# Optimization experiments

Hardware: AMD Instinct MI355X
Metric: run time of the kernel (lower is better)

## Reference

```python
import jax, jax.numpy as jnp
import numpy as np

N = 100000
IN_DIM = 256
HID = 64
HEADS = 2
OUT_DIM = 64
E = 1600000
NEG_SLOPE = 0.2


def gat_conv(x, edge_index, W, att_src, att_dst, bias):
    # PyG GATConv with heads=HEADS, concat=True, add_self_loops=True.
    # x: [N, IN_DIM]; edge_index: [2, E] (row0=src, row1=dst)
    loops = jnp.arange(N, dtype=edge_index.dtype)
    src = jnp.concatenate([edge_index[0], loops])  # [E+N]
    dst = jnp.concatenate([edge_index[1], loops])  # [E+N]
    h = (x @ W).reshape(N, HEADS, HID)             # [N, H, C]
    a_src = jnp.einsum('nhc,hc->nh', h, att_src)   # [N, H]
    a_dst = jnp.einsum('nhc,hc->nh', h, att_dst)   # [N, H]
    e = jax.nn.leaky_relu(a_src[src] + a_dst[dst], NEG_SLOPE)  # [E+N, H]
    # segment softmax over incoming edges of each dst node
    m = jax.ops.segment_max(e, dst, num_segments=N)            # [N, H]
    p = jnp.exp(e - m[dst])
    denom = jax.ops.segment_sum(p, dst, num_segments=N)        # [N, H]
    alpha = p / denom[dst]                                     # [E+N, H]
    msg = h[src] * alpha[:, :, None]                           # [E+N, H, C]
    out = jax.ops.segment_sum(msg, dst, num_segments=N)        # [N, H, C]
    return out.reshape(N, HEADS * HID) + bias


def setup_inputs() -> dict:
    key = jax.random.key(0)
    ks = jax.random.split(key, 12)
    s_in = 1.0 / np.sqrt(IN_DIM)
    s_h = 1.0 / np.sqrt(HID)
    s_fc = 1.0 / np.sqrt(HEADS * HID * 2)
    return {
        'x': jax.random.normal(ks[0], (N, IN_DIM), jnp.float32),
        'edge_index_connected': jax.random.randint(ks[1], (2, E), 0, N, jnp.int32),
        'edge_index_liked': jax.random.randint(ks[2], (2, E), 0, N, jnp.int32),
        'W1': jax.random.normal(ks[3], (IN_DIM, HEADS * HID), jnp.float32) * s_in,
        'att_src1': jax.random.normal(ks[4], (HEADS, HID), jnp.float32) * s_h,
        'att_dst1': jax.random.normal(ks[5], (HEADS, HID), jnp.float32) * s_h,
        'b1': jnp.zeros((HEADS * HID,), jnp.float32),
        'W2': jax.random.normal(ks[6], (IN_DIM, HEADS * HID), jnp.float32) * s_in,
        'att_src2': jax.random.normal(ks[7], (HEADS, HID), jnp.float32) * s_h,
        'att_dst2': jax.random.normal(ks[8], (HEADS, HID), jnp.float32) * s_h,
        'b2': jnp.zeros((HEADS * HID,), jnp.float32),
        'fc_W': jax.random.normal(ks[9], (HEADS * HID * 2, OUT_DIM), jnp.float32) * s_fc,
        'fc_b': jnp.zeros((OUT_DIM,), jnp.float32),
    }


def reference(x, edge_index_connected, edge_index_liked, W1, att_src1, att_dst1, b1,
              W2, att_src2, att_dst2, b2, fc_W, fc_b):
    xc = jax.nn.relu(gat_conv(x, edge_index_connected, W1, att_src1, att_dst1, b1))
    xl = jax.nn.relu(gat_conv(x, edge_index_liked, W2, att_src2, att_dst2, b2))
    x_comb = jnp.concatenate([xc, xl], axis=1)  # [N, 4*HID]
    return x_comb @ fc_W + fc_b
```

## Files before the change

### kernel.cpp

```cpp
#include <hip/hip_runtime.h>
#include <hip/hip_fp16.h>
#include <math.h>

#define NN 100000
#define IN_DIM 256
#define HCH 128
#define OUT_DIM 64
#define EE 1600000
#define NEG_SLOPE 0.2f

#define NB 1024
#define NPB 98
#define CAP 2048

typedef _Float16 half8v __attribute__((ext_vector_type(8)));
typedef _Float16 half4v __attribute__((ext_vector_type(4)));
typedef _Float16 half2v __attribute__((ext_vector_type(2)));
typedef float float4v __attribute__((ext_vector_type(4)));

__device__ __forceinline__ float lrelu(float v) { return v > 0.f ? v : NEG_SLOPE * v; }

__global__ void convw_kernel(const float* __restrict__ W0, const float* __restrict__ W1,
                             const float* __restrict__ fcW,
                             _Float16* __restrict__ wt, _Float16* __restrict__ fcw16)
{
    int i = blockIdx.x * 256 + threadIdx.x;
    if (i < 2 * IN_DIM * HCH) {
        int l = i >> 15, rem = i & 32767;
        int c = rem >> 8, k = rem & 255;
        const float* W = l ? W1 : W0;
        wt[i] = (_Float16)W[(size_t)k * HCH + c];
        return;
    }
    int j = i - 2 * IN_DIM * HCH;
    if (j < 2 * HCH * OUT_DIM) {
        int l = j >> 13, rem = j & 8191;
        int c = rem >> 7, k = rem & 127;
        fcw16[j] = (_Float16)fcW[(size_t)(l * HCH + k) * OUT_DIM + c];
    }
}

__global__ __launch_bounds__(256, 3) void gemm_mfma(
    const float* __restrict__ x, const _Float16* __restrict__ wt,
    const float* __restrict__ attS0, const float* __restrict__ attD0,
    const float* __restrict__ attS1, const float* __restrict__ attD1,
    _Float16* __restrict__ h16, float* __restrict__ a_s, float* __restrict__ a_d, int n)
{
    __shared__ _Float16 smem[64 * 72 + 256 * 72];
    __shared__ float attv[4][128];
    _Float16 (*As)[72] = (_Float16(*)[72])smem;
    _Float16 (*Bs)[72] = (_Float16(*)[72])(smem + 64 * 72);
    const int tid = threadIdx.x;
    const int lane = tid & 63, wave = tid >> 6;
    const int wm = wave & 1, wn = wave >> 1;
    const int q = lane >> 4, r16 = lane & 15;
    const int row0 = blockIdx.x * 64;

    if (tid < 128) {
        attv[0][tid] = attS0[tid]; attv[1][tid] = attD0[tid];
        attv[2][tid] = attS1[tid]; attv[3][tid] = attD1[tid];
    }

    float4v acc[2][8];
#pragma unroll
    for (int i = 0; i < 2; ++i)
#pragma unroll
        for (int j = 0; j < 8; ++j) acc[i][j] = (float4v){0.f, 0.f, 0.f, 0.f};

    const int ar = tid >> 2, aq = tid & 3;
    const bool rok = (row0 + ar) < n;
    for (int kt = 0; kt < IN_DIM; kt += 64) {
        const float* xp = x + (size_t)(row0 + ar) * IN_DIM + kt + aq * 16;
#pragma unroll
        for (int i = 0; i < 4; ++i) {
            float4 v = rok ? *(const float4*)(xp + i * 4) : make_float4(0.f, 0.f, 0.f, 0.f);
            half4v hv = { (_Float16)v.x, (_Float16)v.y, (_Float16)v.z, (_Float16)v.w };
            *(half4v*)&As[ar][aq * 16 + i * 4] = hv;
        }
        const _Float16* wp = wt + (size_t)tid * IN_DIM + kt;
#pragma unroll
        for (int i = 0; i < 8; ++i)
            *(half8v*)&Bs[tid][i * 8] = *(const half8v*)(wp + i * 8);
        __syncthreads();
#pragma unroll
        for (int s = 0; s < 2; ++s) {
            half8v af[2], bf[8];
#pragma unroll
            for (int t = 0; t < 2; ++t)
                af[t] = *(half8v*)&As[wm * 32 + t * 16 + r16][s * 32 + q * 8];
#pragma unroll
            for (int t = 0; t < 8; ++t)
                bf[t] = *(half8v*)&Bs[wn * 128 + t * 16 + r16][s * 32 + q * 8];
#pragma unroll
            for (int mt = 0; mt < 2; ++mt)
#pragma unroll
                for (int nt = 0; nt < 8; ++nt)
                    acc[mt][nt] = __builtin_amdgcn_mfma_f32_16x16x32_f16(
                        af[mt], bf[nt], acc[mt][nt], 0, 0, 0);
        }
        __syncthreads();
    }
    _Float16 (*eb)[264] = (_Float16(*)[264])smem;
#pragma unroll
    for (int mt = 0; mt < 2; ++mt) {
        const int er = wm * 32 + mt * 16 + q * 4;
#pragma unroll
        for (int reg = 0; reg < 4; ++reg)
#pragma unroll
            for (int nt = 0; nt < 8; ++nt)
                eb[er + reg][wn * 128 + nt * 16 + r16] = (_Float16)acc[mt][nt][reg];
    }
    __syncthreads();
    const int r = tid >> 2, qq = tid & 3;
    const int grow = row0 + r;
    if (grow < n) {
        const int l2 = qq >> 1;
        const int hh = qq & 1;
        const float* avS = &attv[l2 * 2 + 0][hh * 64];
        const float* avD = &attv[l2 * 2 + 1][hh * 64];
        _Float16* hout = h16 + (size_t)l2 * NN * HCH + (size_t)grow * HCH + hh * 64;
        float ds = 0.f, dd = 0.f;
#pragma unroll
        for (int i = 0; i < 8; ++i) {
            half8v v = *(half8v*)&eb[r][qq * 64 + i * 8];
            *(half8v*)(hout + i * 8) = v;
#pragma unroll
            for (int j = 0; j < 8; ++j) {
                float f = (float)v[j];
                ds = fmaf(f, avS[i * 8 + j], ds);
                dd = fmaf(f, avD[i * 8 + j], dd);
            }
        }
        a_s[(size_t)l2 * 2 * NN + 2 * grow + hh] = ds;
        a_d[(size_t)l2 * 2 * NN + 2 * grow + hh] = dd;
    }
}

__global__ __launch_bounds__(1024) void bucket_kernel(const int* __restrict__ src,
                                                      const int* __restrict__ dst,
                                                      int* __restrict__ gcursor,
                                                      int* __restrict__ bstore, int e)
{
    __shared__ int hist[NB];
    __shared__ int base[NB];
    const int tid = threadIdx.x;
    const int per = (e + gridDim.x - 1) / gridDim.x;
    const int e0 = blockIdx.x * per;
    const int e1 = min(e, e0 + per);
    for (int i = tid; i < NB; i += 1024) hist[i] = 0;
    __syncthreads();
    for (int i = e0 + tid; i < e1; i += 1024)
        atomicAdd(&hist[dst[i] / NPB], 1);
    __syncthreads();
    for (int b = tid; b < NB; b += 1024) {
        int c = hist[b];
        base[b] = c ? atomicAdd(&gcursor[b], c) : 0;
        hist[b] = 0;
    }
    __syncthreads();
    for (int i = e0 + tid; i < e1; i += 1024) {
        int d = dst[i];
        int s = src[i];
        int b = d / NPB;
        int pos = base[b] + atomicAdd(&hist[b], 1);
        if (pos >= 0 && pos < CAP) bstore[b * CAP + pos] = (s << 7) | (d - b * NPB);
    }
}

__global__ __launch_bounds__(256) void sort_kernel(
    const int* __restrict__ gcursor, int* __restrict__ bstore,
    int* __restrict__ gstart, int* __restrict__ gend, int n)
{
    __shared__ int raw[CAP];
    __shared__ int sorted[CAP];
    __shared__ int curs[128];
    __shared__ int scanbuf[128];
    const int tid = threadIdx.x;
    const int b = blockIdx.x;
    const int node0 = b * NPB;
    const int nnode = min(NPB, n - node0);
    if (nnode <= 0) return;
    int cnt = gcursor[b];
    cnt = cnt < 0 ? 0 : (cnt > CAP ? CAP : cnt);

    for (int i = tid; i < cnt; i += 256) raw[i] = bstore[b * CAP + i];
    if (tid < 128) curs[tid] = 0;
    __syncthreads();
    for (int i = tid; i < cnt; i += 256) atomicAdd(&curs[raw[i] & 127], 1);
    __syncthreads();
    if (tid < 128) scanbuf[tid] = curs[tid];
    __syncthreads();
    for (int off = 1; off < 128; off <<= 1) {
        int v = 0;
        if (tid < 128) { v = scanbuf[tid]; if (tid >= off) v += scanbuf[tid - off]; }
        __syncthreads();
        if (tid < 128) scanbuf[tid] = v;
        __syncthreads();
    }
    if (tid < 128) {
        int ex = tid ? scanbuf[tid - 1] : 0;
        curs[tid] = ex;
        if (tid < nnode) {
            gstart[node0 + tid] = b * CAP + ex;
            gend[node0 + tid] = b * CAP + scanbuf[tid];
        }
    }
    __syncthreads();
    for (int i = tid; i < cnt; i += 256) {
        int item = raw[i];
        int pos = atomicAdd(&curs[item & 127], 1);
        if (pos >= 0 && pos < CAP) sorted[pos] = item >> 7;
    }
    __syncthreads();
    for (int i = tid; i < cnt; i += 256) bstore[b * CAP + i] = sorted[i];
}

__global__ __launch_bounds__(256) void agg_kernel(
    const _Float16* __restrict__ h16, const float2* __restrict__ a_s,
    const float2* __restrict__ a_d, const int* __restrict__ gstart,
    const int* __restrict__ gend, const int* __restrict__ ssort,
    const float* __restrict__ bias, _Float16* __restrict__ xc16, int n)
{
    __shared__ float2 sh[4][2][64];
    const int wid = threadIdx.x >> 6, lane = threadIdx.x & 63;
    const int wbase = (blockIdx.x * 4 + wid) * 4;
    const int cl = lane & 15;
    const int w  = lane >> 4;
    const int hh = cl >> 3;
    const float2* myh = &sh[wid][hh][0];

    float bv[8];
#pragma unroll
    for (int j = 0; j < 8; ++j) bv[j] = bias[cl * 8 + j];

    for (int ni = 0; ni < 4; ++ni) {
        const int node = wbase + ni;
        const bool valid = node < n;
        const int nn = valid ? node : 0;
        int start = gstart[nn], end = gend[nn];
        start = start < 0 ? 0 : (start > NB * CAP ? NB * CAP : start);
        end = end < start ? start : (end > NB * CAP ? NB * CAP : end);
        const float2 ad = a_d[nn];
        const float2 asn = a_s[nn];

        float acc[8] = {0.f, 0.f, 0.f, 0.f, 0.f, 0.f, 0.f, 0.f};
        float s0 = 0.f, s1 = 0.f;

        for (int base = start; base < end; base += 64) {
            const int j = base + lane;
            const int cnt = min(64, end - base);
            float p0 = 0.f, p1 = 0.f;
            int s = 0;
            if (j < end) {
                s = ssort[j];
                if ((unsigned)s >= (unsigned)n) s = 0;
                float2 a = a_s[s];
                p0 = __expf(lrelu(a.x + ad.x));
                p1 = __expf(lrelu(a.y + ad.y));
            }
            s0 += p0;
            s1 += p1;
            sh[wid][0][lane] = make_float2(__int_as_float(s), p0);
            sh[wid][1][lane] = make_float2(__int_as_float(s), p1);
            __builtin_amdgcn_wave_barrier();
            const int cnt4 = (cnt + 3) & ~3;
            for (int t = 0; t < cnt4; t += 4) {
                const float2 e = myh[t + w];
                const half8v hv = *(const half8v*)(
                    h16 + (size_t)__float_as_int(e.x) * HCH + cl * 8);
#pragma unroll
                for (int j2 = 0; j2 < 8; ++j2)
                    acc[j2] = fmaf(e.y, (float)hv[j2], acc[j2]);
            }
            __builtin_amdgcn_wave_barrier();
        }
        const float ps0 = __expf(lrelu(asn.x + ad.x));
        const float ps1 = __expf(lrelu(asn.y + ad.y));
        if (w == 0) {
            const half8v hv = *(const half8v*)(h16 + (size_t)nn * HCH + cl * 8);
            const float pl = hh ? ps1 : ps0;
#pragma unroll
            for (int j2 = 0; j2 < 8; ++j2)
                acc[j2] = fmaf(pl, (float)hv[j2], acc[j2]);
        }
        if (lane == 0) { s0 += ps0; s1 += ps1; }
#pragma unroll
        for (int j2 = 0; j2 < 8; ++j2) {
            acc[j2] += __shfl_xor(acc[j2], 16, 64);
            acc[j2] += __shfl_xor(acc[j2], 32, 64);
        }
#pragma unroll
        for (int m = 32; m >= 1; m >>= 1) {
            s0 += __shfl_xor(s0, m, 64);
            s1 += __shfl_xor(s1, m, 64);
        }
        if (valid && lane < 16) {
            const float inv = 1.f / (hh ? s1 : s0);
            half8v o;
#pragma unroll
            for (int j2 = 0; j2 < 8; ++j2)
                o[j2] = (_Float16)fmaxf(acc[j2] * inv + bv[j2], 0.f);
            *(half8v*)(xc16 + (size_t)node * HCH + cl * 8) = o;
        }
    }
}

__global__ __launch_bounds__(256) void fc_mfma(const _Float16* __restrict__ xc16,
                                               const _Float16* __restrict__ fw16,
                                               const float* __restrict__ fcb,
                                               float* __restrict__ out, int n, int beta)
{
    __shared__ _Float16 axs[64][136];
    const int tid = threadIdx.x;
    const int lane = tid & 63, wave = tid >> 6;
    const int q = lane >> 4, r16 = lane & 15;
    const int row0 = blockIdx.x * 64;

#pragma unroll
    for (int i = 0; i < 4; ++i) {
        const int idx = i * 256 + tid;
        const int row = idx >> 4;
        const int kg = (idx & 15) * 8;
        half8v v = { 0, 0, 0, 0, 0, 0, 0, 0 };
        if (row0 + row < n)
            v = *(const half8v*)(xc16 + (size_t)(row0 + row) * HCH + kg);
        *(half8v*)&axs[row][kg] = v;
    }
    __syncthreads();

    float4v acc[4];
#pragma unroll
    for (int i = 0; i < 4; ++i) acc[i] = (float4v){0.f, 0.f, 0.f, 0.f};
#pragma unroll
    for (int s = 0; s < 4; ++s) {
        const half8v af = *(half8v*)&axs[wave * 16 + r16][s * 32 + q * 8];
#pragma unroll
        for (int nt = 0; nt < 4; ++nt) {
            const half8v bf =
                *(const half8v*)(fw16 + (size_t)(nt * 16 + r16) * HCH + s * 32 + q * 8);
            acc[nt] = __builtin_amdgcn_mfma_f32_16x16x32_f16(af, bf, acc[nt], 0, 0, 0);
        }
    }
#pragma unroll
    for (int nt = 0; nt < 4; ++nt) {
        const int col = nt * 16 + r16;
#pragma unroll
        for (int reg = 0; reg < 4; ++reg) {
            const int row = row0 + wave * 16 + q * 4 + reg;
            if (row < n) {
                float v = acc[nt][reg];
                if (beta) v += out[(size_t)row * OUT_DIM + col];
                else v += fcb[col];
                out[(size_t)row * OUT_DIM + col] = v;
            }
        }
    }
}

extern "C" void kernel_launch(void* const* d_in, const int* in_sizes, int n_in,
                              void* d_out, int out_size, void* d_ws, size_t ws_size,
                              hipStream_t stream)
{
    const float* x = (const float*)d_in[0];
    const int* ei[2] = { (const int*)d_in[1], (const int*)d_in[2] };
    const float* W[2] = { (const float*)d_in[3], (const float*)d_in[7] };
    const float* attS[2] = { (const float*)d_in[4], (const float*)d_in[8] };
    const float* attD[2] = { (const float*)d_in[5], (const float*)d_in[9] };
    const float* bias[2] = { (const float*)d_in[6], (const float*)d_in[10] };
    const float* fcW = (const float*)d_in[11];
    const float* fcb = (const float*)d_in[12];
    float* out = (float*)d_out;

    char* p = (char*)d_ws;
    size_t need = 0;
    auto carve = [&](size_t bytes) {
        char* r = p;
        size_t b = (bytes + 255) & ~(size_t)255;
        p += b;
        need += b;
        return r;
    };
    _Float16* h16 = (_Float16*)carve((size_t)2 * NN * HCH * 2);
    _Float16* xc16 = (_Float16*)carve((size_t)NN * HCH * 2);
    _Float16* wt = (_Float16*)carve((size_t)2 * IN_DIM * HCH * 2);
    _Float16* fcw16 = (_Float16*)carve((size_t)2 * HCH * OUT_DIM * 2);
    float* a_s = (float*)carve((size_t)2 * NN * 8);
    float* a_d = (float*)carve((size_t)2 * NN * 8);
    int* gcursor = (int*)carve((size_t)NB * 4);
    int* bstore = (int*)carve((size_t)NB * CAP * 4);
    int* gstart = (int*)carve((size_t)NN * 4);
    int* gend = (int*)carve((size_t)NN * 4);
    if (need > ws_size) return;

    const int gemm_blocks = (NN + 63) / 64;
    const int agg_blocks = (NN + 15) / 16;
    const int conv_total = 2 * IN_DIM * HCH + 2 * HCH * OUT_DIM;

    convw_kernel<<<(conv_total + 255) / 256, 256, 0, stream>>>(W[0], W[1], fcW, wt, fcw16);

    gemm_mfma<<<gemm_blocks, 256, 0, stream>>>(x, wt, attS[0], attD[0], attS[1], attD[1],
                                               h16, a_s, a_d, NN);

    for (int layer = 0; layer < 2; ++layer) {
        hipMemsetAsync(gcursor, 0, (size_t)NB * 4, stream);
        bucket_kernel<<<256, 1024, 0, stream>>>(ei[layer], ei[layer] + EE, gcursor, bstore, EE);
        sort_kernel<<<NB, 256, 0, stream>>>(gcursor, bstore, gstart, gend, NN);
        agg_kernel<<<agg_blocks, 256, 0, stream>>>(
            h16 + (size_t)layer * NN * HCH,
            (const float2*)a_s + (size_t)layer * NN,
            (const float2*)a_d + (size_t)layer * NN,
            gstart, gend, bstore, bias[layer], xc16, NN);
        fc_mfma<<<gemm_blocks, 256, 0, stream>>>(xc16, fcw16 + (size_t)layer * HCH * OUT_DIM,
                                                 fcb, out, NN, layer);
    }
}
```

Before: 498.5 us.

## Batch both GAT layers per launch, pack fp16 attention weights, single fused FC

Both edge sets are now bucketed, sorted and aggregated in single launches using blockIdx.y as the layer index, with separate workspace per layer. The aggregation writes both layers into one 256-wide buffer, so a single FC GEMM over K=256 replaces two FC passes and the read-modify-write of the output. The inner aggregation loop packs source index and fp16 pair weights into 8-byte records, handles two edges per step with packed fdot2, and computes the denominator inside the same loop. This cuts launch count and serial dependencies and doubles the parallel work per launch, at the cost of more workspace and fp16 rounding of the softmax numerators.

After: 464.9 us. 1.07x faster.

```diff
diff --git a/kernel.cpp b/kernel.cpp
--- a/kernel.cpp
+++ b/kernel.cpp
@@ -16,13 +16,17 @@
 typedef _Float16 half8v __attribute__((ext_vector_type(8)));
 typedef _Float16 half4v __attribute__((ext_vector_type(4)));
 typedef _Float16 half2v __attribute__((ext_vector_type(2)));
+typedef __fp16 fp16x2 __attribute__((ext_vector_type(2)));
 typedef float float4v __attribute__((ext_vector_type(4)));
+typedef unsigned int u32;
+
+union H2U { u32 u; fp16x2 h; };
 
 __device__ __forceinline__ float lrelu(float v) { return v > 0.f ? v : NEG_SLOPE * v; }
 
 __global__ void convw_kernel(const float* __restrict__ W0, const float* __restrict__ W1,
                              const float* __restrict__ fcW,
-                             _Float16* __restrict__ wt, _Float16* __restrict__ fcw16)
+                             _Float16* __restrict__ wt, _Float16* __restrict__ fcw2)
 {
     int i = blockIdx.x * 256 + threadIdx.x;
     if (i < 2 * IN_DIM * HCH) {
@@ -33,10 +37,9 @@
         return;
     }
     int j = i - 2 * IN_DIM * HCH;
-    if (j < 2 * HCH * OUT_DIM) {
-        int l = j >> 13, rem = j & 8191;
-        int c = rem >> 7, k = rem & 127;
-        fcw16[j] = (_Float16)fcW[(size_t)(l * HCH + k) * OUT_DIM + c];
+    if (j < 256 * OUT_DIM) {
+        int c = j >> 8, k = j & 255;
+        fcw2[j] = (_Float16)fcW[(size_t)k * OUT_DIM + c];
     }
 }
 
@@ -136,13 +139,19 @@
     }
 }
 
-__global__ __launch_bounds__(1024) void bucket_kernel(const int* __restrict__ src,
-                                                      const int* __restrict__ dst,
+__global__ __launch_bounds__(1024) void bucket_kernel(const int* __restrict__ ei0,
+                                                      const int* __restrict__ ei1,
                                                       int* __restrict__ gcursor,
                                                       int* __restrict__ bstore, int e)
 {
     __shared__ int hist[NB];
     __shared__ int base[NB];
+    const int lay = blockIdx.y;
+    const int* src = lay ? ei1 : ei0;
+    const int* dst = src + e;
+    int* gcur = gcursor + lay * NB;
+    int* bst = bstore + (size_t)lay * NB * CAP;
+
     const int tid = threadIdx.x;
     const int per = (e + gridDim.x - 1) / gridDim.x;
     const int e0 = blockIdx.x * per;
@@ -154,7 +163,7 @@
     __syncthreads();
     for (int b = tid; b < NB; b += 1024) {
         int c = hist[b];
-        base[b] = c ? atomicAdd(&gcursor[b], c) : 0;
+        base[b] = c ? atomicAdd(&gcur[b], c) : 0;
         hist[b] = 0;
     }
     __syncthreads();
@@ -163,7 +172,7 @@
         int s = src[i];
         int b = d / NPB;
         int pos = base[b] + atomicAdd(&hist[b], 1);
-        if (pos >= 0 && pos < CAP) bstore[b * CAP + pos] = (s << 7) | (d - b * NPB);
+        if (pos >= 0 && pos < CAP) bst[b * CAP + pos] = (s << 7) | (d - b * NPB);
     }
 }
 
@@ -175,15 +184,21 @@
     __shared__ int sorted[CAP];
     __shared__ int curs[128];
     __shared__ int scanbuf[128];
+    const int lay = blockIdx.y;
+    const int* gcur = gcursor + lay * NB;
+    int* bst = bstore + (size_t)lay * NB * CAP;
+    int* gs = gstart + (size_t)lay * NN;
+    int* ge = gend + (size_t)lay * NN;
+
     const int tid = threadIdx.x;
     const int b = blockIdx.x;
     const int node0 = b * NPB;
     const int nnode = min(NPB, n - node0);
     if (nnode <= 0) return;
-    int cnt = gcursor[b];
+    int cnt = gcur[b];
     cnt = cnt < 0 ? 0 : (cnt > CAP ? CAP : cnt);
 
-    for (int i = tid; i < cnt; i += 256) raw[i] = bstore[b * CAP + i];
+    for (int i = tid; i < cnt; i += 256) raw[i] = bst[b * CAP + i];
     if (tid < 128) curs[tid] = 0;
     __syncthreads();
     for (int i = tid; i < cnt; i += 256) atomicAdd(&curs[raw[i] & 127], 1);
@@ -201,8 +216,8 @@
         int ex = tid ? scanbuf[tid - 1] : 0;
         curs[tid] = ex;
         if (tid < nnode) {
-            gstart[node0 + tid] = b * CAP + ex;
-            gend[node0 + tid] = b * CAP + scanbuf[tid];
+            gs[node0 + tid] = b * CAP + ex;
+            ge[node0 + tid] = b * CAP + scanbuf[tid];
         }
     }
     __syncthreads();
@@ -212,22 +227,33 @@
         if (pos >= 0 && pos < CAP) sorted[pos] = item >> 7;
     }
     __syncthreads();
-    for (int i = tid; i < cnt; i += 256) bstore[b * CAP + i] = sorted[i];
+    for (int i = tid; i < cnt; i += 256) bst[b * CAP + i] = sorted[i];
 }
 
 __global__ __launch_bounds__(256) void agg_kernel(
     const _Float16* __restrict__ h16, const float2* __restrict__ a_s,
     const float2* __restrict__ a_d, const int* __restrict__ gstart,
-    const int* __restrict__ gend, const int* __restrict__ ssort,
-    const float* __restrict__ bias, _Float16* __restrict__ xc16, int n)
-{
-    __shared__ float2 sh[4][2][64];
+    const int* __restrict__ gend, const int* __restrict__ bstore,
+    const float* __restrict__ bias0, const float* __restrict__ bias1,
+    _Float16* __restrict__ xc16, int n)
+{
+    __shared__ __align__(16) uint2 sh[4][64];
+    const int lay = blockIdx.y;
+    const _Float16* hL = h16 + (size_t)lay * NN * HCH;
+    const float2* asL = a_s + (size_t)lay * NN;
+    const float2* adL = a_d + (size_t)lay * NN;
+    const int* gsL = gstart + (size_t)lay * NN;
+    const int* geL = gend + (size_t)lay * NN;
+    const int* ssort = bstore + (size_t)lay * NB * CAP;
+    const float* bias = lay ? bias1 : bias0;
+
     const int wid = threadIdx.x >> 6, lane = threadIdx.x & 63;
     const int wbase = (blockIdx.x * 4 + wid) * 4;
     const int cl = lane & 15;
-    const int w  = lane >> 4;
+    const int w2 = lane >> 4;
     const int hh = cl >> 3;
-    const float2* myh = &sh[wid][hh][0];
+    const u32 psel = hh ? 0x07060302u : 0x05040100u;
+    const fp16x2 one2 = { (__fp16)1.f, (__fp16)1.f };
 
     float bv[8];
 #pragma unroll
@@ -237,14 +263,14 @@
         const int node = wbase + ni;
         const bool valid = node < n;
         const int nn = valid ? node : 0;
-        int start = gstart[nn], end = gend[nn];
+        int start = gsL[nn], end = geL[nn];
         start = start < 0 ? 0 : (start > NB * CAP ? NB * CAP : start);
         end = end < start ? start : (end > NB * CAP ? NB * CAP : end);
-        const float2 ad = a_d[nn];
-        const float2 asn = a_s[nn];
+        const float2 ad = adL[nn];
+        const float2 asn = asL[nn];
 
         float acc[8] = {0.f, 0.f, 0.f, 0.f, 0.f, 0.f, 0.f, 0.f};
-        float s0 = 0.f, s1 = 0.f;
+        float den = 0.f;
 
         for (int base = start; base < end; base += 64) {
             const int j = base + lane;
@@ -254,76 +280,80 @@
             if (j < end) {
                 s = ssort[j];
                 if ((unsigned)s >= (unsigned)n) s = 0;
-                float2 a = a_s[s];
+                float2 a = asL[s];
                 p0 = __expf(lrelu(a.x + ad.x));
                 p1 = __expf(lrelu(a.y + ad.y));
             }
-            s0 += p0;
-            s1 += p1;
-            sh[wid][0][lane] = make_float2(__int_as_float(s), p0);
-            sh[wid][1][lane] = make_float2(__int_as_float(s), p1);
+            H2U pk; pk.h = __builtin_amdgcn_cvt_pkrtz(p0, p1);
+            sh[wid][lane] = make_uint2((u32)s, pk.u);
             __builtin_amdgcn_wave_barrier();
-            const int cnt4 = (cnt + 3) & ~3;
-            for (int t = 0; t < cnt4; t += 4) {
-                const float2 e = myh[t + w];
-                const half8v hv = *(const half8v*)(
-                    h16 + (size_t)__float_as_int(e.x) * HCH + cl * 8);
-#pragma unroll
-                for (int j2 = 0; j2 < 8; ++j2)
-                    acc[j2] = fmaf(e.y, (float)hv[j2], acc[j2]);
+            const int cnt8 = (cnt + 7) & ~7;
+            for (int t = 0; t < cnt8; t += 8) {
+                const uint4 rec = *(const uint4*)&sh[wid][t + 2 * w2];
+                H2U pph; pph.u = __builtin_amdgcn_perm(rec.w, rec.y, psel);
+                const half8v hv0 = *(const half8v*)(hL + ((rec.x << 7) | (u32)(cl << 3)));
+                const half8v hv1 = *(const half8v*)(hL + ((rec.z << 7) | (u32)(cl << 3)));
+                const u32* ap = (const u32*)&hv0;
+                const u32* bp = (const u32*)&hv1;
+#pragma unroll
+                for (int d2 = 0; d2 < 4; ++d2) {
+                    H2U pe, po;
+                    pe.u = __builtin_amdgcn_perm(bp[d2], ap[d2], 0x05040100u);
+                    po.u = __builtin_amdgcn_perm(bp[d2], ap[d2], 0x07060302u);
+                    acc[2 * d2]     = __builtin_amdgcn_fdot2(pe.h, pph.h, acc[2 * d2], false);
+                    acc[2 * d2 + 1] = __builtin_amdgcn_fdot2(po.h, pph.h, acc[2 * d2 + 1], false);
+                }
+                den = __builtin_amdgcn_fdot2(pph.h, one2, den, false);
             }
             __builtin_amdgcn_wave_barrier();
         }
         const float ps0 = __expf(lrelu(asn.x + ad.x));
         const float ps1 = __expf(lrelu(asn.y + ad.y));
-        if (w == 0) {
-            const half8v hv = *(const half8v*)(h16 + (size_t)nn * HCH + cl * 8);
+        if (w2 == 0) {
+            const half8v hv = *(const half8v*)(hL + (((u32)nn << 7) | (u32)(cl << 3)));
             const float pl = hh ? ps1 : ps0;
 #pragma unroll
             for (int j2 = 0; j2 < 8; ++j2)
                 acc[j2] = fmaf(pl, (float)hv[j2], acc[j2]);
-        }
-        if (lane == 0) { s0 += ps0; s1 += ps1; }
+            den += pl;
+        }
 #pragma unroll
         for (int j2 = 0; j2 < 8; ++j2) {
             acc[j2] += __shfl_xor(acc[j2], 16, 64);
             acc[j2] += __shfl_xor(acc[j2], 32, 64);
         }
-#pragma unroll
-        for (int m = 32; m >= 1; m >>= 1) {
-            s0 += __shfl_xor(s0, m, 64);
-            s1 += __shfl_xor(s1, m, 64);
-        }
+        den += __shfl_xor(den, 16, 64);
+        den += __shfl_xor(den, 32, 64);
         if (valid && lane < 16) {
-            const float inv = 1.f / (hh ? s1 : s0);
+            const float inv = 1.f / den;
             half8v o;
 #pragma unroll
             for (int j2 = 0; j2 < 8; ++j2)
                 o[j2] = (_Float16)fmaxf(acc[j2] * inv + bv[j2], 0.f);
-            *(half8v*)(xc16 + (size_t)node * HCH + cl * 8) = o;
+            *(half8v*)(xc16 + (size_t)node * 256 + lay * HCH + cl * 8) = o;
         }
     }
 }
 
 __global__ __launch_bounds__(256) void fc_mfma(const _Float16* __restrict__ xc16,
-                                               const _Float16* __restrict__ fw16,
+                                               const _Float16* __restrict__ fw2,
                                                const float* __restrict__ fcb,
-                                               float* __restrict__ out, int n, int beta)
-{
-    __shared__ _Float16 axs[64][136];
+                                               float* __restrict__ out, int n)
+{
+    __shared__ _Float16 axs[64][264];
     const int tid = threadIdx.x;
     const int lane = tid & 63, wave = tid >> 6;
     const int q = lane >> 4, r16 = lane & 15;
     const int row0 = blockIdx.x * 64;
 
 #pragma unroll
-    for (int i = 0; i < 4; ++i) {
+    for (int i = 0; i < 8; ++i) {
         const int idx = i * 256 + tid;
-        const int row = idx >> 4;
-        const int kg = (idx & 15) * 8;
+        const int row = idx >> 5;
+        const int kg = (idx & 31) * 8;
         half8v v = { 0, 0, 0, 0, 0, 0, 0, 0 };
         if (row0 + row < n)
-            v = *(const half8v*)(xc16 + (size_t)(row0 + row) * HCH + kg);
+            v = *(const half8v*)(xc16 + (size_t)(row0 + row) * 256 + kg);
         *(half8v*)&axs[row][kg] = v;
     }
     __syncthreads();
@@ -332,12 +362,12 @@
 #pragma unroll
     for (int i = 0; i < 4; ++i) acc[i] = (float4v){0.f, 0.f, 0.f, 0.f};
 #pragma unroll
-    for (int s = 0; s < 4; ++s) {
+    for (int s = 0; s < 8; ++s) {
         const half8v af = *(half8v*)&axs[wave * 16 + r16][s * 32 + q * 8];
 #pragma unroll
         for (int nt = 0; nt < 4; ++nt) {
             const half8v bf =
-                *(const half8v*)(fw16 + (size_t)(nt * 16 + r16) * HCH + s * 32 + q * 8);
+                *(const half8v*)(fw2 + (size_t)(nt * 16 + r16) * 256 + s * 32 + q * 8);
             acc[nt] = __builtin_amdgcn_mfma_f32_16x16x32_f16(af, bf, acc[nt], 0, 0, 0);
         }
     }
@@ -347,12 +377,8 @@
 #pragma unroll
         for (int reg = 0; reg < 4; ++reg) {
             const int row = row0 + wave * 16 + q * 4 + reg;
-            if (row < n) {
-                float v = acc[nt][reg];
-                if (beta) v += out[(size_t)row * OUT_DIM + col];
-                else v += fcb[col];
-                out[(size_t)row * OUT_DIM + col] = v;
-            }
+            if (row < n)
+                out[(size_t)row * OUT_DIM + col] = acc[nt][reg] + fcb[col];
         }
     }
 }
@@ -381,36 +407,31 @@
         return r;
     };
     _Float16* h16 = (_Float16*)carve((size_t)2 * NN * HCH * 2);
-    _Float16* xc16 = (_Float16*)carve((size_t)NN * HCH * 2);
+    _Float16* xc16 = (_Float16*)carve((size_t)NN * 256 * 2);
     _Float16* wt = (_Float16*)carve((size_t)2 * IN_DIM * HCH * 2);
-    _Float16* fcw16 = (_Float16*)carve((size_t)2 * HCH * OUT_DIM * 2);
+    _Float16* fcw2 = (_Float16*)carve((size_t)256 * OUT_DIM * 2);
     float* a_s = (float*)carve((size_t)2 * NN * 8);
     float* a_d = (float*)carve((size_t)2 * NN * 8);
-    int* gcursor = (int*)carve((size_t)NB * 4);
-    int* bstore = (int*)carve((size_t)NB * CAP * 4);
-    int* gstart = (int*)carve((size_t)NN * 4);
-    int* gend = (int*)carve((size_t)NN * 4);
+    int* gcursor = (int*)carve((size_t)2 * NB * 4);
+    int* bstore = (int*)carve((size_t)2 * NB * CAP * 4);
+    int* gstart = (int*)carve((size_t)2 * NN * 4);
+    int* gend = (int*)carve((size_t)2 * NN * 4);
     if (need > ws_size) return;
 
     const int gemm_blocks = (NN + 63) / 64;
     const int agg_blocks = (NN + 15) / 16;
-    const int conv_total = 2 * IN_DIM * HCH + 2 * HCH * OUT_DIM;
-
-    convw_kernel<<<(conv_total + 255) / 256, 256, 0, stream>>>(W[0], W[1], fcW, wt, fcw16);
+    const int conv_total = 2 * IN_DIM * HCH + 256 * OUT_DIM;
+
+    convw_kernel<<<(conv_total + 255) / 256, 256, 0, stream>>>(W[0], W[1], fcW, wt, fcw2);
 
     gemm_mfma<<<gemm_blocks, 256, 0, stream>>>(x, wt, attS[0], attD[0], attS[1], attD[1],
                                                h16, a_s, a_d, NN);
 
-    for (int layer = 0; layer < 2; ++layer) {
-        hipMemsetAsync(gcursor, 0, (size_t)NB * 4, stream);
-        bucket_kernel<<<256, 1024, 0, stream>>>(ei[layer], ei[layer] + EE, gcursor, bstore, EE);
-        sort_kernel<<<NB, 256, 0, stream>>>(gcursor, bstore, gstart, gend, NN);
-        agg_kernel<<<agg_blocks, 256, 0, stream>>>(
-            h16 + (size_t)layer * NN * HCH,
-            (const float2*)a_s + (size_t)layer * NN,
-            (const float2*)a_d + (size_t)layer * NN,
-            gstart, gend, bstore, bias[layer], xc16, NN);
-        fc_mfma<<<gemm_blocks, 256, 0, stream>>>(xc16, fcw16 + (size_t)layer * HCH * OUT_DIM,
-                                                 fcb, out, NN, layer);
-    }
-}
+    (void)hipMemsetAsync(gcursor, 0, (size_t)2 * NB * 4, stream);
+    bucket_kernel<<<dim3(256, 2), 1024, 0, stream>>>(ei[0], ei[1], gcursor, bstore, EE);
+    sort_kernel<<<dim3(NB, 2), 256, 0, stream>>>(gcursor, bstore, gstart, gend, NN);
+    agg_kernel<<<dim3(agg_blocks, 2), 256, 0, stream>>>(
+        h16, (const float2*)a_s, (const float2*)a_d,
+        gstart, gend, bstore, bias[0], bias[1], xc16, NN);
+    fc_mfma<<<gemm_blocks, 256, 0, stream>>>(xc16, fcw2, fcb, out, NN);
+}
```
